# Optimization experiments

Measured on AMD Instinct MI355X. Metric: run time of the kernel, lower is better.

## Reference

```python
import math
import jax, jax.numpy as jnp
import numpy as np

B, L, D, H = 4, 2048, 1024, 16
DH = D // H  # head dim = 64
PAD_LEN = 128  # trailing padded positions


def setup_inputs() -> dict:
    key = jax.random.key(0)
    ks = jax.random.split(key, 12)
    q = jax.random.normal(ks[0], (B, L, D), dtype=jnp.float32)
    k = jax.random.normal(ks[1], (B, L, D), dtype=jnp.float32)
    v = jax.random.normal(ks[2], (B, L, D), dtype=jnp.float32)
    # additive causal mask: 0 on/below diagonal, -inf above
    causal = jnp.triu(jnp.ones((L, L), dtype=bool), k=1)
    att_mask = jnp.where(causal, -jnp.inf, 0.0).astype(jnp.float32)
    # boolean pad mask over key positions: last PAD_LEN positions are padding
    pad_mask = (jnp.arange(L) >= (L - PAD_LEN))[None, :].repeat(B, axis=0)
    s = 0.02
    params = {
        'w_q': jax.random.normal(ks[3], (D, D), jnp.float32) * s,
        'b_q': jnp.zeros((D,), jnp.float32),
        'w_k': jax.random.normal(ks[4], (D, D), jnp.float32) * s,
        'b_k': jnp.zeros((D,), jnp.float32),
        'w_v': jax.random.normal(ks[5], (D, D), jnp.float32) * s,
        'b_v': jnp.zeros((D,), jnp.float32),
        'w_out': jax.random.normal(ks[6], (D, D), jnp.float32) * s,
        'b_out': jnp.zeros((D,), jnp.float32),
    }
    return {'q': q, 'k': k, 'v': v, 'att_mask': att_mask, 'pad_mask': pad_mask, **params}


def reference(q, k, v, att_mask, pad_mask, w_q, b_q, w_k, b_k, w_v, b_v, w_out, b_out):
    b, l, d = q.shape
    qp = q @ w_q.T + b_q
    kp = k @ w_k.T + b_k  # computed but unused below: source stacks q for k and v (faithful)
    vp = v @ w_v.T + b_v  # computed but unused below (faithful to source bug)
    # split(ndim//nhead, dim=2) + stack(dim=1) == reshape + transpose -> [B,H,L,DH]
    qh = qp.reshape(b, l, H, DH).transpose(0, 2, 1, 3)
    kh = qh  # source: torch.stack(q, ...) used for k
    vh = qh  # source: torch.stack(q, ...) used for v
    att = jnp.einsum('bhqd,bhkd->bhqk', qh, kh) / math.sqrt(DH)
    att = att + att_mask  # broadcast [L,L] over [B,H,L,L]
    # pad_mask [B,L] over keys, broadcast across heads and query positions
    att = jnp.where(pad_mask[:, None, None, :], -jnp.inf, att)
    p = jax.nn.softmax(att, axis=-1)
    o = jnp.einsum('bhqk,bhkd->bhqd', p, vh)
    o = o.transpose(0, 2, 1, 3).reshape(b, l, d)
    return o @ w_out.T + b_out
```

## Files before the change

### kernel.cpp

```cpp
#include <hip/hip_runtime.h>
#include <math.h>


typedef __attribute__((ext_vector_type(8))) short bf16x8;
typedef __attribute__((ext_vector_type(8))) unsigned short u16x8;
typedef __attribute__((ext_vector_type(4))) float f32x4;
typedef __attribute__((ext_vector_type(2))) unsigned int u32x2;

#define MFMA16(a, b, c) __builtin_amdgcn_mfma_f32_16x16x32_bf16(a, b, c, 0, 0, 0)

#define GLDS16(g, l) __builtin_amdgcn_global_load_lds(                        \
    (const __attribute__((address_space(1))) unsigned int*)(g),               \
    (__attribute__((address_space(3))) unsigned int*)(l), 16, 0, 0)

__device__ __forceinline__ unsigned short f2bf(float f) {
    union { float f; unsigned int u; } x; x.f = f;
    unsigned int u = x.u + 0x7fffu + ((x.u >> 16) & 1u);
    return (unsigned short)(u >> 16);
}

__device__ __forceinline__ unsigned int pack_bf16(float lo, float hi) {
    union { float f; unsigned int u; } a, b;
    a.f = lo; b.f = hi;
    return __builtin_amdgcn_perm(b.u + 0x8000u, a.u + 0x8000u, 0x07060302u);
}

__global__ __launch_bounds__(256) void cast_bf16(const float* __restrict__ s,
                                                 unsigned short* __restrict__ d, int n) {
    int i = (blockIdx.x * 256 + threadIdx.x) * 8;
    if (i >= n) return;
    f32x4 a = *(const f32x4*)(s + i);
    f32x4 b = *(const f32x4*)(s + i + 4);
    u16x8 o;
    o[0] = f2bf(a[0]); o[1] = f2bf(a[1]); o[2] = f2bf(a[2]); o[3] = f2bf(a[3]);
    o[4] = f2bf(b[0]); o[5] = f2bf(b[1]); o[6] = f2bf(b[2]); o[7] = f2bf(b[3]);
    *(u16x8*)(d + i) = o;
}

__global__ __launch_bounds__(256) void gemm_bt(
    const unsigned short* __restrict__ A,
    const unsigned short* __restrict__ Bw,
    const float* __restrict__ bias,
    unsigned short* __restrict__ Cbf,
    float* __restrict__ Cf,
    int M, int N, int K, int mode)
{
    __shared__ __align__(16) short lA[128 * 64];
    __shared__ __align__(16) short lB[128 * 64];
    const int tid = threadIdx.x;
    const int lane = tid & 63, w = tid >> 6;
    const int quad = lane >> 4, l16 = lane & 15;
    const int m0 = blockIdx.y * 128, n0 = blockIdx.x * 128;
    const int wm = (w >> 1) * 64, wn = (w & 1) * 64;

    const int r8 = lane >> 3;
    const int ch = (lane & 7) ^ r8;
    const unsigned short* Ag = A  + (size_t)(m0 + w * 32 + r8) * K + ch * 8;
    const unsigned short* Bg = Bw + (size_t)(n0 + w * 32 + r8) * K + ch * 8;

    f32x4 acc[4][4];
#pragma unroll
    for (int i = 0; i < 4; ++i)
#pragma unroll
        for (int j = 0; j < 4; ++j) acc[i][j] = (f32x4){0.f, 0.f, 0.f, 0.f};

    for (int k0 = 0; k0 < K; k0 += 64) {
        __syncthreads();
#pragma unroll
        for (int j = 0; j < 4; ++j) {
            GLDS16(Ag + (size_t)j * 8 * K + k0, &lA[(w * 32 + j * 8) * 64]);
            GLDS16(Bg + (size_t)j * 8 * K + k0, &lB[(w * 32 + j * 8) * 64]);
        }
        __syncthreads();
#pragma unroll
        for (int ks = 0; ks < 2; ++ks) {
            const int kc = (ks << 2) + quad;
            const int sw = (kc ^ (l16 & 7)) * 8;
            bf16x8 af[4], bfr[4];
#pragma unroll
            for (int i = 0; i < 4; ++i)
                af[i] = *(bf16x8*)&lA[(wm + i * 16 + l16) * 64 + sw];
#pragma unroll
            for (int j = 0; j < 4; ++j)
                bfr[j] = *(bf16x8*)&lB[(wn + j * 16 + l16) * 64 + sw];
#pragma unroll
            for (int i = 0; i < 4; ++i)
#pragma unroll
                for (int j = 0; j < 4; ++j)
                    acc[i][j] = MFMA16(af[i], bfr[j], acc[i][j]);
        }
    }

#pragma unroll
    for (int i = 0; i < 4; ++i)
#pragma unroll
        for (int j = 0; j < 4; ++j) {
            int col = n0 + wn + j * 16 + l16;
            float bv = bias[col];
#pragma unroll
            for (int r = 0; r < 4; ++r) {
                int row = m0 + wm + i * 16 + quad * 4 + r;
                float v = acc[i][j][r] + bv;
                if (mode == 0) {
                    int b = row >> 11, l = row & 2047;
                    int h = col >> 6, dh = col & 63;
                    Cbf[(((size_t)(b * 16 + h) * 2048) + l) * 64 + dh] = f2bf(v);
                } else {
                    Cf[(size_t)row * N + col] = v;
                }
            }
        }
}

__global__ __launch_bounds__(256, 4) void attn_kernel(
    const unsigned short* __restrict__ qh,
    unsigned short* __restrict__ obf)
{
    __shared__ __align__(16) short kv [64 * 72];
    __shared__ __align__(16) short kvT[64 * 72];
    __shared__ __align__(16) short pls[128 * 72];
    const int tid = threadIdx.x;
    const int lane = tid & 63, w = tid >> 6;
    const int quad = lane >> 4, l16 = lane & 15;
    const int bh = blockIdx.x & 63;
    const int g = blockIdx.x >> 6;
    const int ga = g >> 2, gb = g & 3;
    const int qt2 = (ga == 0) ? 15 - gb : (ga == 1) ? 8 + gb : (ga == 2) ? 7 - gb : gb;
    const int rbase = qt2 << 7;
    const unsigned short* __restrict__ base = qh + ((size_t)bh << 17);

    bf16x8 bq[2][2];
    int rmin[2];
#pragma unroll
    for (int s = 0; s < 2; ++s) {
        rmin[s] = rbase + w * 32 + s * 16;
        const unsigned short* qrow = base + (size_t)(rmin[s] + l16) * 64 + quad * 8;
        bq[s][0] = *(const bf16x8*)qrow;
        bq[s][1] = *(const bf16x8*)(qrow + 32);
    }

    float lsum[2] = {0.f, 0.f};
    f32x4 oacc[2][4];
#pragma unroll
    for (int s = 0; s < 2; ++s)
#pragma unroll
        for (int t = 0; t < 4; ++t) oacc[s][t] = (f32x4){0.f, 0.f, 0.f, 0.f};

    const int nkt = min(2 * qt2 + 2, 30);
    const float c = 0.18033688011f;
    short* pw0 = pls + (w * 2 + 0) * (16 * 72);
    short* pw1 = pls + (w * 2 + 1) * (16 * 72);

    for (int kt = 0; kt < nkt; ++kt) {
        const int kb = kt << 6;
        __syncthreads();
        const unsigned short* src = base + (size_t)(kb + lane) * 64 + w * 16;
        u16x8 d0 = *(const u16x8*)src;
        u16x8 d1 = *(const u16x8*)(src + 8);
        *(u16x8*)&kv[lane * 72 + w * 16]     = d0;
        *(u16x8*)&kv[lane * 72 + w * 16 + 8] = d1;
#pragma unroll
        for (int j = 0; j < 8; ++j) kvT[(w * 16 + j) * 72 + lane]     = d0[j];
#pragma unroll
        for (int j = 0; j < 8; ++j) kvT[(w * 16 + 8 + j) * 72 + lane] = d1[j];
        __syncthreads();

        const bool act0 = (kb <= rmin[0] + 15);
        const bool act1 = (kb <= rmin[1] + 15);
        const bool dg0 = (kb + 63 > rmin[0]);
        const bool dg1 = (kb + 63 > rmin[1]);

#pragma unroll
        for (int t = 0; t < 4; ++t) {
            bf16x8 fk0 = *(bf16x8*)&kv[(t * 16 + l16) * 72 + quad * 8];
            bf16x8 fk1 = *(bf16x8*)&kv[(t * 16 + l16) * 72 + 32 + quad * 8];
            const int keyb = kb + t * 16 + 4 * quad;
#pragma unroll
            for (int s = 0; s < 2; ++s) {
                if (!(s ? act1 : act0)) continue;
                f32x4 sv = (f32x4){0.f, 0.f, 0.f, 0.f};
                sv = MFMA16(fk0, bq[s][0], sv);
                sv = MFMA16(fk1, bq[s][1], sv);
                const bool dgs = s ? dg1 : dg0;
                const int qg = rmin[s] + l16;
                float p[4];
#pragma unroll
                for (int r = 0; r < 4; ++r) {
                    float pv = exp2f(sv[r] * c);
                    if (dgs && (keyb + r > qg)) pv = 0.f;
                    p[r] = pv;
                    lsum[s] += pv;
                }
                u32x2 pk;
                pk[0] = pack_bf16(p[0], p[1]);
                pk[1] = pack_bf16(p[2], p[3]);
                short* pws = s ? pw1 : pw0;
                *(u32x2*)&pws[l16 * 72 + t * 16 + 4 * quad] = pk;
            }
        }

#pragma unroll
        for (int ks = 0; ks < 2; ++ks) {
            bf16x8 bp0, bp1;
            if (act0) bp0 = *(bf16x8*)&pw0[l16 * 72 + ks * 32 + quad * 8];
            if (act1) bp1 = *(bf16x8*)&pw1[l16 * 72 + ks * 32 + quad * 8];
#pragma unroll
            for (int t2 = 0; t2 < 4; ++t2) {
                bf16x8 av = *(bf16x8*)&kvT[(t2 * 16 + l16) * 72 + ks * 32 + quad * 8];
                if (act0) oacc[0][t2] = MFMA16(av, bp0, oacc[0][t2]);
                if (act1) oacc[1][t2] = MFMA16(av, bp1, oacc[1][t2]);
            }
        }
    }

    const int b = bh >> 4, h = bh & 15;
#pragma unroll
    for (int s = 0; s < 2; ++s) {
        float rs = lsum[s];
        rs += __shfl_xor(rs, 16);
        rs += __shfl_xor(rs, 32);
        const float inv = 1.f / rs;
        unsigned short* orow = obf + ((size_t)(b * 2048 + rmin[s] + l16)) * 1024
                             + h * 64 + 4 * quad;
#pragma unroll
        for (int t2 = 0; t2 < 4; ++t2) {
            u32x2 pk;
            pk[0] = pack_bf16(oacc[s][t2][0] * inv, oacc[s][t2][1] * inv);
            pk[1] = pack_bf16(oacc[s][t2][2] * inv, oacc[s][t2][3] * inv);
            *(u32x2*)(orow + t2 * 16) = pk;
        }
    }
}

extern "C" void kernel_launch(void* const* d_in, const int* in_sizes, int n_in,
                              void* d_out, int out_size, void* d_ws, size_t ws_size,
                              hipStream_t stream) {
    const float* q     = (const float*)d_in[0];
    const float* w_q   = (const float*)d_in[5];
    const float* b_q   = (const float*)d_in[6];
    const float* w_out = (const float*)d_in[11];
    const float* b_out = (const float*)d_in[12];
    float* out = (float*)d_out;

    char* ws = (char*)d_ws;
    unsigned short* a_bf   = (unsigned short*)ws;
    unsigned short* wq_bf  = (unsigned short*)(ws + (16u << 20));
    unsigned short* wo_bf  = (unsigned short*)(ws + (18u << 20));
    unsigned short* qheads = (unsigned short*)(ws + (20u << 20));
    unsigned short* o_bf   = a_bf;

    hipLaunchKernelGGL(cast_bf16, dim3(4096), dim3(256), 0, stream, q, a_bf, 8388608);
    hipLaunchKernelGGL(cast_bf16, dim3(512),  dim3(256), 0, stream, w_q, wq_bf, 1048576);
    hipLaunchKernelGGL(cast_bf16, dim3(512),  dim3(256), 0, stream, w_out, wo_bf, 1048576);

    hipLaunchKernelGGL(gemm_bt, dim3(8, 64), dim3(256), 0, stream,
                       a_bf, wq_bf, b_q, qheads, (float*)nullptr, 8192, 1024, 1024, 0);
    hipLaunchKernelGGL(attn_kernel, dim3(1024), dim3(256), 0, stream, qheads, o_bf);
    hipLaunchKernelGGL(gemm_bt, dim3(8, 64), dim3(256), 0, stream,
                       o_bf, wo_bf, b_out, (unsigned short*)nullptr, out, 8192, 1024, 1024, 1);
}
```

Baseline: 289.2 us.

## Double-buffer LDS tiles in GEMM and merge the three cast kernels

After: 286.9 us. About the same (-0.8%).

```diff
diff --git a/kernel.cpp b/kernel.cpp
--- a/kernel.cpp
+++ b/kernel.cpp
@@ -25,10 +25,16 @@
     return __builtin_amdgcn_perm(b.u + 0x8000u, a.u + 0x8000u, 0x07060302u);
 }
 
-__global__ __launch_bounds__(256) void cast_bf16(const float* __restrict__ s,
-                                                 unsigned short* __restrict__ d, int n) {
-    int i = (blockIdx.x * 256 + threadIdx.x) * 8;
-    if (i >= n) return;
+__global__ __launch_bounds__(256) void cast3_bf16(
+    const float* __restrict__ s0, unsigned short* __restrict__ d0,
+    const float* __restrict__ s1, unsigned short* __restrict__ d1,
+    const float* __restrict__ s2, unsigned short* __restrict__ d2)
+{
+    const float* s; unsigned short* d; int i;
+    int blk = blockIdx.x;
+    if (blk < 4096)      { s = s0; d = d0; i = (blk * 256 + threadIdx.x) * 8; }
+    else if (blk < 4608) { s = s1; d = d1; i = ((blk - 4096) * 256 + threadIdx.x) * 8; }
+    else                 { s = s2; d = d2; i = ((blk - 4608) * 256 + threadIdx.x) * 8; }
     f32x4 a = *(const f32x4*)(s + i);
     f32x4 b = *(const f32x4*)(s + i + 4);
     u16x8 o;
@@ -45,8 +51,8 @@
     float* __restrict__ Cf,
     int M, int N, int K, int mode)
 {
-    __shared__ __align__(16) short lA[128 * 64];
-    __shared__ __align__(16) short lB[128 * 64];
+    __shared__ __align__(16) short lA[2][128 * 64];
+    __shared__ __align__(16) short lB[2][128 * 64];
     const int tid = threadIdx.x;
     const int lane = tid & 63, w = tid >> 6;
     const int quad = lane >> 4, l16 = lane & 15;
@@ -64,14 +70,14 @@
 #pragma unroll
         for (int j = 0; j < 4; ++j) acc[i][j] = (f32x4){0.f, 0.f, 0.f, 0.f};
 
-    for (int k0 = 0; k0 < K; k0 += 64) {
-        __syncthreads();
+    auto prefetch = [&](int k0, int buf) {
 #pragma unroll
         for (int j = 0; j < 4; ++j) {
-            GLDS16(Ag + (size_t)j * 8 * K + k0, &lA[(w * 32 + j * 8) * 64]);
-            GLDS16(Bg + (size_t)j * 8 * K + k0, &lB[(w * 32 + j * 8) * 64]);
-        }
-        __syncthreads();
+            GLDS16(Ag + (size_t)j * 8 * K + k0, &lA[buf][(w * 32 + j * 8) * 64]);
+            GLDS16(Bg + (size_t)j * 8 * K + k0, &lB[buf][(w * 32 + j * 8) * 64]);
+        }
+    };
+    auto compute = [&](int buf) {
 #pragma unroll
         for (int ks = 0; ks < 2; ++ks) {
             const int kc = (ks << 2) + quad;
@@ -79,16 +85,27 @@
             bf16x8 af[4], bfr[4];
 #pragma unroll
             for (int i = 0; i < 4; ++i)
-                af[i] = *(bf16x8*)&lA[(wm + i * 16 + l16) * 64 + sw];
+                af[i] = *(bf16x8*)&lA[buf][(wm + i * 16 + l16) * 64 + sw];
 #pragma unroll
             for (int j = 0; j < 4; ++j)
-                bfr[j] = *(bf16x8*)&lB[(wn + j * 16 + l16) * 64 + sw];
+                bfr[j] = *(bf16x8*)&lB[buf][(wn + j * 16 + l16) * 64 + sw];
 #pragma unroll
             for (int i = 0; i < 4; ++i)
 #pragma unroll
                 for (int j = 0; j < 4; ++j)
                     acc[i][j] = MFMA16(af[i], bfr[j], acc[i][j]);
         }
+    };
+
+    const int niter = K >> 6;
+    prefetch(0, 0);
+    for (int k = 0; k < niter; k += 2) {
+        __syncthreads();
+        if (k + 1 < niter) prefetch((k + 1) << 6, 1);
+        compute(0);
+        __syncthreads();
+        if (k + 2 < niter) prefetch((k + 2) << 6, 0);
+        if (k + 1 < niter) compute(1);
     }
 
 #pragma unroll
@@ -249,9 +266,8 @@
     unsigned short* qheads = (unsigned short*)(ws + (20u << 20));
     unsigned short* o_bf   = a_bf;
 
-    hipLaunchKernelGGL(cast_bf16, dim3(4096), dim3(256), 0, stream, q, a_bf, 8388608);
-    hipLaunchKernelGGL(cast_bf16, dim3(512),  dim3(256), 0, stream, w_q, wq_bf, 1048576);
-    hipLaunchKernelGGL(cast_bf16, dim3(512),  dim3(256), 0, stream, w_out, wo_bf, 1048576);
+    hipLaunchKernelGGL(cast3_bf16, dim3(5120), dim3(256), 0, stream,
+                       q, a_bf, w_q, wq_bf, w_out, wo_bf);
 
     hipLaunchKernelGGL(gemm_bt, dim3(8, 64), dim3(256), 0, stream,
                        a_bf, wq_bf, b_q, qheads, (float*)nullptr, 8192, 1024, 1024, 0);
```
